# Kernel optimization log

Hardware: AMD Instinct MI355X
Metric: run time of the kernel (lower is better)

## Reference

```python
import jax, jax.numpy as jnp
import numpy as np

D_MODEL = 1024
N_HEADS = 16
HDIM = D_MODEL // N_HEADS
IMP_EPS = 1e-6


def setup_inputs() -> dict:
    key = jax.random.key(0)
    ks = jax.random.split(key, 7)
    B, T_q, T_kv, N_s = 2, 2048, 256, 16
    scale = 1.0 / np.sqrt(D_MODEL)
    return {
        "query": jax.random.normal(ks[0], (B, T_q, D_MODEL), dtype=jnp.float32),
        "key_value": jax.random.normal(ks[1], (B, T_kv, N_s, D_MODEL), dtype=jnp.float32),
        "imp_weights": jax.random.uniform(ks[2], (B, N_s), dtype=jnp.float32),
        "W_q": jax.random.normal(ks[3], (D_MODEL, D_MODEL), dtype=jnp.float32) * scale,
        "W_k": jax.random.normal(ks[4], (D_MODEL, D_MODEL), dtype=jnp.float32) * scale,
        "W_v": jax.random.normal(ks[5], (D_MODEL, D_MODEL), dtype=jnp.float32) * scale,
        "W_o": jax.random.normal(ks[6], (D_MODEL, D_MODEL), dtype=jnp.float32) * scale,
    }


def _split_heads(x):
    # [B, T, D] -> [B, h, T, d]
    B, T, _ = x.shape
    return x.reshape(B, T, N_HEADS, HDIM).transpose(0, 2, 1, 3)


def reference(query, key_value, imp_weights, W_q, W_k, W_v, W_o):
    # CAU_MultiheadCrossAttention.forward with 4D key_value (sensor axis).
    B, T_q, D = query.shape
    _, T_kv, N_s, _ = key_value.shape
    kv = key_value.reshape(B, T_kv * N_s, D)  # flatten sensor axis into source length S

    qh = _split_heads(query @ W_q.T)   # [B,h,T_q,d]  (nn.Linear: x @ W.T)
    kh = _split_heads(kv @ W_k.T)      # [B,h,S,d]
    vh = _split_heads(kv @ W_v.T)      # [B,h,S,d]

    # importance: [B,N_s] -> tiled over T_kv -> [B, S], log-clamped additive mask
    imp_full = jnp.broadcast_to(imp_weights[:, None, :], (B, T_kv, N_s)).reshape(B, T_kv * N_s)
    log_imp = jnp.log(jnp.clip(imp_full, IMP_EPS, None)).astype(qh.dtype)  # [B,S]

    scores = jnp.einsum("bhqd,bhkd->bhqk", qh, kh) / np.sqrt(HDIM).astype(np.float32)
    scores = scores + log_imp[:, None, None, :]
    attn = jax.nn.softmax(scores, axis=-1)
    y = jnp.einsum("bhqk,bhkd->bhqd", attn, vh)  # [B,h,T_q,d]

    y = y.transpose(0, 2, 1, 3).reshape(B, T_q, D)  # merge heads
    return y @ W_o.T
```

## Files before the change

kernel.cpp:

```cpp
#include <hip/hip_runtime.h>
#include <hip/hip_bf16.h>

typedef __bf16    bf16x8_t __attribute__((ext_vector_type(8)));
typedef __bf16    bf16x4_t __attribute__((ext_vector_type(4)));
typedef float     f32x4_t  __attribute__((ext_vector_type(4)));
typedef _Float16  f16x8_t  __attribute__((ext_vector_type(8)));

static __device__ __forceinline__ f32x4_t mfma16(bf16x8_t a, bf16x8_t b, f32x4_t c) {
    return __builtin_amdgcn_mfma_f32_16x16x32_bf16(a, b, c, 0, 0, 0);
}

static __device__ __forceinline__ float redsum16(float v) {
#pragma unroll
    for (int off = 1; off < 16; off <<= 1) v += __shfl_xor(v, off);
    return v;
}

static __device__ __forceinline__ void async16(const __bf16* g, __bf16* l) {
    __builtin_amdgcn_global_load_lds(
        (const __attribute__((address_space(1))) unsigned int*)g,
        (__attribute__((address_space(3))) unsigned int*)l, 16, 0, 0);
}

__global__ __launch_bounds__(256) void f2b_multi(const float* __restrict__ q,
                                                 const float* __restrict__ kv,
                                                 const float* __restrict__ wq,
                                                 const float* __restrict__ wk,
                                                 const float* __restrict__ wv,
                                                 const float* __restrict__ wo,
                                                 __bf16* __restrict__ qb,
                                                 __bf16* __restrict__ kvb,
                                                 __bf16* __restrict__ wqb,
                                                 __bf16* __restrict__ wkvb,
                                                 __bf16* __restrict__ wob,
                                                 float qscale) {
    int i = blockIdx.x * 256 + threadIdx.x;
    const float* src; __bf16* dst; int base; float scale = 1.0f;
    if (i < 1048576)      { src = q;  dst = qb;   base = 0; }
    else if (i < 3145728) { src = kv; dst = kvb;  base = 1048576; }
    else if (i < 3407872) { src = wq; dst = wqb;  base = 3145728; scale = qscale; }
    else if (i < 3670016) { src = wk; dst = wkvb; base = 3407872; }
    else if (i < 3932160) { src = wv; dst = wkvb + 1048576; base = 3670016; }
    else                  { src = wo; dst = wob;  base = 3932160; }
    int j = i - base;
    float4 v = reinterpret_cast<const float4*>(src)[j];
    bf16x4_t o;
    o[0] = (__bf16)(v.x * scale); o[1] = (__bf16)(v.y * scale);
    o[2] = (__bf16)(v.z * scale); o[3] = (__bf16)(v.w * scale);
    reinterpret_cast<bf16x4_t*>(dst)[j] = o;
}

__global__ __launch_bounds__(256) void proj_kernel(const __bf16* __restrict__ qb,
                                                   const __bf16* __restrict__ wqb,
                                                   const __bf16* __restrict__ kvb,
                                                   const __bf16* __restrict__ wkvb,
                                                   __bf16* __restrict__ Qp,
                                                   __bf16* __restrict__ Khd,
                                                   __bf16* __restrict__ Vhd,
                                                   const float* __restrict__ imp) {
    __shared__ __bf16 As[128 * 32];
    __shared__ __bf16 Bs[128 * 32];
    __shared__ __bf16 Es[2][4096];

    const int gid = blockIdx.x;
    const __bf16 *A, *B;
    long m0, n0;
    int mode;
    if (gid < 256) {
        m0 = (long)(gid >> 3) * 128; n0 = (long)(gid & 7) * 128;
        A = qb; B = wqb; mode = 0;
    } else {
        int g2 = gid - 256;
        m0 = (long)(g2 >> 4) * 128; n0 = (long)(g2 & 15) * 128;
        A = kvb; B = wkvb; mode = (n0 < 1024) ? 1 : 2;
    }

    const int t    = threadIdx.x;
    const int w    = t >> 6;
    const int lane = t & 63;
    const int quad = lane >> 4;
    const int mn   = lane & 15;
    const int wm   = (w & 1) * 64;
    const int wn   = (w >> 1) * 64;

    const int  srow = t >> 2;
    const int  scol = (t & 3) * 8;
    const __bf16* gA = A + (m0 + srow) * 1024 + scol;
    const __bf16* gB = B + (n0 + srow) * 1024 + scol;

    f32x4_t acc[4][4];
#pragma unroll
    for (int i = 0; i < 4; i++)
#pragma unroll
        for (int j = 0; j < 4; j++) acc[i][j] = (f32x4_t){0.f, 0.f, 0.f, 0.f};

    for (int k0 = 0; k0 < 1024; k0 += 32) {
        __syncthreads();
        async16(gA + k0,              &As[t * 8]);
        async16(gA + 64 * 1024 + k0,  &As[2048 + t * 8]);
        async16(gB + k0,              &Bs[t * 8]);
        async16(gB + 64 * 1024 + k0,  &Bs[2048 + t * 8]);
        __syncthreads();

        bf16x8_t af[4], bf[4];
#pragma unroll
        for (int i = 0; i < 4; i++)
            af[i] = *(const bf16x8_t*)&As[(wm + i * 16 + mn) * 32 + quad * 8];
#pragma unroll
        for (int j = 0; j < 4; j++)
            bf[j] = *(const bf16x8_t*)&Bs[(wn + j * 16 + mn) * 32 + quad * 8];
#pragma unroll
        for (int i = 0; i < 4; i++)
#pragma unroll
            for (int j = 0; j < 4; j++) acc[i][j] = mfma16(af[i], bf[j], acc[i][j]);
    }

    __syncthreads();
    __bf16* stg = (w == 0) ? As : (w == 1) ? Bs : Es[w - 2];

    if (mode != 2) {
#pragma unroll
        for (int i = 0; i < 4; i++)
#pragma unroll
            for (int j = 0; j < 4; j++)
#pragma unroll
                for (int r = 0; r < 4; r++) {
                    int sl = i * 16 + quad * 4 + r;
                    int d  = j * 16 + mn;
                    stg[sl * 64 + (((d >> 3) ^ (sl & 7)) * 8) + (d & 7)] =
                        (__bf16)acc[i][j][r];
                }
    } else {
        const int b_ = (int)((m0 + wm) >> 12);
#pragma unroll
        for (int r = 0; r < 4; r++) {
            float scl = fmaxf(imp[b_ * 16 + quad * 4 + r], 1e-6f);
#pragma unroll
            for (int j = 0; j < 4; j++) {
                bf16x4_t pk;
#pragma unroll
                for (int i = 0; i < 4; i++) pk[i] = (__bf16)(acc[i][j][r] * scl);
                int d  = j * 16 + mn;
                int p0 = (quad * 4 + r) * 4;
                *(bf16x4_t*)&stg[d * 64 + (((p0 >> 3) ^ (d & 7)) * 8) + (p0 & 7)] = pk;
            }
        }
    }

    if (mode == 0) {
        __bf16* Cg = Qp + (m0 + wm) * 1024 + (n0 + wn);
#pragma unroll
        for (int it = 0; it < 8; it++) {
            int rowL = it * 8 + (lane >> 3);
            int cb   = lane & 7;
            bf16x8_t vv = *(const bf16x8_t*)&stg[rowL * 64 + ((cb ^ (rowL & 7)) * 8)];
            *(bf16x8_t*)&Cg[(long)rowL * 1024 + cb * 8] = vv;
        }
    } else {
        const int b_    = (int)((m0 + wm) >> 12);
        const int sbase = (int)((m0 + wm) & 4095);
        __bf16* dst;
        if (mode == 1) {
            int h_ = (int)((n0 + wn) >> 6);
            dst = Khd + (long)(b_ * 16 + h_) * 262144 + (long)sbase * 64;
        } else {
            int h_ = (int)((n0 + wn) >> 6) - 16;
            dst = Vhd + (long)(b_ * 16 + h_) * 262144 + (long)(sbase >> 6) * 4096;
        }
#pragma unroll
        for (int it = 0; it < 8; it++) {
            int rowL = it * 8 + (lane >> 3);
            int cb   = lane & 7;
            bf16x8_t vv = *(const bf16x8_t*)&stg[rowL * 64 + ((cb ^ (rowL & 7)) * 8)];
            *(bf16x8_t*)&dst[rowL * 64 + cb * 8] = vv;
        }
    }
}

__global__ __launch_bounds__(256, 4) void attn_kernel(const __bf16* __restrict__ Qp,
                                                      const __bf16* __restrict__ Kh,
                                                      const __bf16* __restrict__ Vh,
                                                      const float* __restrict__ imp,
                                                      _Float16* __restrict__ Op,
                                                      float* __restrict__ Lp) {
    const int gid = blockIdx.x;
    const int qt  = (gid >> 3) & 15;
    const int sp  = (gid >> 7) & 1;
    const int bh  = ((gid >> 8) << 3) | (gid & 7);
    const int b   = bh >> 4;
    const int h   = bh & 15;
    const int t    = threadIdx.x;
    const int w    = t >> 6;
    const int lane = t & 63;
    const int quad = lane >> 4;
    const int mn   = lane & 15;

    __shared__ __bf16 Ks[2][64 * 64];
    __shared__ __bf16 Vs[64 * 64];
    __shared__ __bf16 Ps[4][32 * 64];

    const long qrow0 = (long)b * 2048 + qt * 128 + w * 32;
    const __bf16* Kb = Kh + (long)bh * 262144;
    const __bf16* Vb = Vh + (long)bh * 262144;

    const int r8 = lane >> 3;
    const int cs = (lane & 7) ^ r8;
    const int soff    = r8 * 64 + cs * 8;
    const int srcoff0 = (0 * 4 + w) * 512 + soff;
    const int srcoff1 = (1 * 4 + w) * 512 + soff;

    bf16x8_t aq[2][2];
#pragma unroll
    for (int rt = 0; rt < 2; rt++)
#pragma unroll
        for (int x = 0; x < 2; x++)
            aq[rt][x] = *(const bf16x8_t*)&Qp[(qrow0 + rt * 16 + mn) * 1024 + h * 64 + x * 32 + quad * 8];

    const float impc = fmaxf(imp[b * 16 + mn], 1e-6f);

    float lpart[2][4];
    f32x4_t o[2][4];
#pragma unroll
    for (int rt = 0; rt < 2; rt++)
#pragma unroll
        for (int r = 0; r < 4; r++) lpart[rt][r] = 0.f;
#pragma unroll
    for (int rt = 0; rt < 2; rt++)
#pragma unroll
        for (int dt = 0; dt < 4; dt++) o[rt][dt] = (f32x4_t){0.f, 0.f, 0.f, 0.f};

    const int st0 = sp * 32;

    async16(Kb + (long)st0 * 4096 + srcoff0, &Ks[0][(0 * 4 + w) * 512]);
    async16(Kb + (long)st0 * 4096 + srcoff1, &Ks[0][(1 * 4 + w) * 512]);

    for (int it = 0; it < 32; ++it) {
        const int st  = st0 + it;
        const int cur = it & 1;

        __syncthreads();

        async16(Vb + (long)st * 4096 + srcoff0,       &Vs[(0 * 4 + w) * 512]);
        async16(Vb + (long)st * 4096 + srcoff1,       &Vs[(1 * 4 + w) * 512]);
        async16(Kb + (long)(st + 1) * 4096 + srcoff0, &Ks[cur ^ 1][(0 * 4 + w) * 512]);
        async16(Kb + (long)(st + 1) * 4096 + srcoff1, &Ks[cur ^ 1][(1 * 4 + w) * 512]);

        const __bf16* Kc = &Ks[cur][0];
        f32x4_t sc[2][4];
#pragma unroll
        for (int rt = 0; rt < 2; rt++)
#pragma unroll
            for (int ct = 0; ct < 4; ct++) sc[rt][ct] = (f32x4_t){0.f, 0.f, 0.f, 0.f};
#pragma unroll
        for (int ct = 0; ct < 4; ct++) {
            int s  = ct * 16 + mn;
            int c0 = (quad ^ (s & 7)) * 8;
            bf16x8_t bk0 = *(const bf16x8_t*)&Kc[s * 64 + c0];
            bf16x8_t bk1 = *(const bf16x8_t*)&Kc[s * 64 + (c0 ^ 32)];
#pragma unroll
            for (int rt = 0; rt < 2; rt++) {
                sc[rt][ct] = mfma16(aq[rt][0], bk0, sc[rt][ct]);
                sc[rt][ct] = mfma16(aq[rt][1], bk1, sc[rt][ct]);
            }
        }

#pragma unroll
        for (int rt = 0; rt < 2; rt++)
#pragma unroll
            for (int r = 0; r < 4; r++) {
                float p0 = __builtin_amdgcn_exp2f(sc[rt][0][r]);
                float p1 = __builtin_amdgcn_exp2f(sc[rt][1][r]);
                float p2 = __builtin_amdgcn_exp2f(sc[rt][2][r]);
                float p3 = __builtin_amdgcn_exp2f(sc[rt][3][r]);
                lpart[rt][r] += (p0 + p1) + (p2 + p3);
                bf16x4_t pk;
                pk[0] = (__bf16)p0; pk[1] = (__bf16)p1;
                pk[2] = (__bf16)p2; pk[3] = (__bf16)p3;
                int row = rt * 16 + quad * 4 + r;
                *(bf16x4_t*)&Ps[w][row * 64 + (((mn >> 1) ^ (row & 7)) * 8) + (mn & 1) * 4] = pk;
            }

        __syncthreads();

        {
            bf16x8_t bv0[4], bv1[4];
#pragma unroll
            for (int dt = 0; dt < 4; dt++) {
                int d  = dt * 16 + mn;
                int c0 = (quad ^ (d & 7)) * 8;
                bv0[dt] = *(const bf16x8_t*)&Vs[d * 64 + c0];
                bv1[dt] = *(const bf16x8_t*)&Vs[d * 64 + (c0 ^ 32)];
            }
#pragma unroll
            for (int rt = 0; rt < 2; rt++) {
                int arow = rt * 16 + mn;
                bf16x8_t ap0 = *(const bf16x8_t*)&Ps[w][arow * 64 + ((quad ^ (mn & 7)) * 8)];
                bf16x8_t ap1 = *(const bf16x8_t*)&Ps[w][arow * 64 + (((4 + quad) ^ (mn & 7)) * 8)];
#pragma unroll
                for (int dt = 0; dt < 4; dt++) {
                    o[rt][dt] = mfma16(ap0, bv0[dt], o[rt][dt]);
                    o[rt][dt] = mfma16(ap1, bv1[dt], o[rt][dt]);
                }
            }
        }
    }

#pragma unroll
    for (int rt = 0; rt < 2; rt++)
#pragma unroll
        for (int r = 0; r < 4; r++) {
            float l = redsum16(lpart[rt][r] * impc);
            long row = qrow0 + rt * 16 + quad * 4 + r;
            if (mn == 0) Lp[((long)sp * 4096 + row) * 16 + h] = l;
#pragma unroll
            for (int dt = 0; dt < 4; dt++)
                Op[((long)sp * 4096 + row) * 1024 + h * 64 + dt * 16 + mn] =
                    (_Float16)o[rt][dt][r];
        }
}

__global__ __launch_bounds__(256) void combine_kernel(const _Float16* __restrict__ Op,
                                                      const float* __restrict__ Lp,
                                                      __bf16* __restrict__ Y) {
    int tid = blockIdx.x * 256 + threadIdx.x;
    int row = tid >> 7;
    int cg  = tid & 127;
    int h   = cg >> 3;
    f16x8_t o0 = *(const f16x8_t*)&Op[(long)row * 1024 + cg * 8];
    f16x8_t o1 = *(const f16x8_t*)&Op[(long)(4096 + row) * 1024 + cg * 8];
    float inv = 1.0f / (Lp[row * 16 + h] + Lp[(4096 + row) * 16 + h]);
    bf16x8_t y;
#pragma unroll
    for (int j = 0; j < 8; j++) y[j] = (__bf16)(((float)o0[j] + (float)o1[j]) * inv);
    *(bf16x8_t*)&Y[(long)row * 1024 + cg * 8] = y;
}

__global__ __launch_bounds__(256) void gemm_out_kernel(const __bf16* __restrict__ A,
                                                       const __bf16* __restrict__ B,
                                                       float* __restrict__ P) {
    __shared__ __bf16 As[128 * 32];
    __shared__ __bf16 Bs[128 * 32];

    const int  kh = blockIdx.x >> 3;
    const long n0 = (long)(blockIdx.x & 7) * 128;
    const long m0 = (long)blockIdx.y * 128;
    const int  kb = kh * 512;
    float* C = P + (long)kh * 4194304;

    const int t    = threadIdx.x;
    const int w    = t >> 6;
    const int lane = t & 63;
    const int quad = lane >> 4;
    const int mn   = lane & 15;
    const int wm   = (w & 1) * 64;
    const int wn   = (w >> 1) * 64;

    const int  srow = t >> 2;
    const int  scol = (t & 3) * 8;
    const __bf16* gA = A + (m0 + srow) * 1024 + kb + scol;
    const __bf16* gB = B + (n0 + srow) * 1024 + kb + scol;

    f32x4_t acc[4][4];
#pragma unroll
    for (int i = 0; i < 4; i++)
#pragma unroll
        for (int j = 0; j < 4; j++) acc[i][j] = (f32x4_t){0.f, 0.f, 0.f, 0.f};

    for (int k0 = 0; k0 < 512; k0 += 32) {
        __syncthreads();
        async16(gA + k0,             &As[t * 8]);
        async16(gA + 64 * 1024 + k0, &As[2048 + t * 8]);
        async16(gB + k0,             &Bs[t * 8]);
        async16(gB + 64 * 1024 + k0, &Bs[2048 + t * 8]);
        __syncthreads();

        bf16x8_t af[4], bf[4];
#pragma unroll
        for (int i = 0; i < 4; i++)
            af[i] = *(const bf16x8_t*)&As[(wm + i * 16 + mn) * 32 + quad * 8];
#pragma unroll
        for (int j = 0; j < 4; j++)
            bf[j] = *(const bf16x8_t*)&Bs[(wn + j * 16 + mn) * 32 + quad * 8];
#pragma unroll
        for (int i = 0; i < 4; i++)
#pragma unroll
            for (int j = 0; j < 4; j++) acc[i][j] = mfma16(af[i], bf[j], acc[i][j]);
    }

#pragma unroll
    for (int i = 0; i < 4; i++)
#pragma unroll
        for (int j = 0; j < 4; j++)
#pragma unroll
            for (int r = 0; r < 4; r++) {
                long row = m0 + wm + i * 16 + quad * 4 + r;
                long col = n0 + wn + j * 16 + mn;
                C[row * 1024 + col] = acc[i][j][r];
            }
}

__global__ __launch_bounds__(256) void combine2_kernel(const float* __restrict__ P0,
                                                       const float* __restrict__ P1,
                                                       float* __restrict__ out) {
    int i = blockIdx.x * 256 + threadIdx.x;
    float4 a = reinterpret_cast<const float4*>(P0)[i];
    float4 b = reinterpret_cast<const float4*>(P1)[i];
    float4 c; c.x = a.x + b.x; c.y = a.y + b.y; c.z = a.z + b.z; c.w = a.w + b.w;
    reinterpret_cast<float4*>(out)[i] = c;
}

extern "C" void kernel_launch(void* const* d_in, const int* in_sizes, int n_in,
                              void* d_out, int out_size, void* d_ws, size_t ws_size,
                              hipStream_t stream) {
    const float* q_f  = (const float*)d_in[0];
    const float* kv_f = (const float*)d_in[1];
    const float* imp  = (const float*)d_in[2];
    const float* wq_f = (const float*)d_in[3];
    const float* wk_f = (const float*)d_in[4];
    const float* wv_f = (const float*)d_in[5];
    const float* wo_f = (const float*)d_in[6];

    char* ws = (char*)d_ws;
    const size_t MB = 1ull << 20;
    __bf16*   qb    = (__bf16*)(ws + 0);
    __bf16*   kvb   = (__bf16*)(ws + 8 * MB);
    __bf16*   wqb   = (__bf16*)(ws + 24 * MB);
    __bf16*   wkvb  = (__bf16*)(ws + 26 * MB);
    _Float16* Opart = (_Float16*)(ws + 0);
    float*    Lpart = (float*)(ws + 16 * MB);
    __bf16*   Yb    = (__bf16*)(ws + 17 * MB);
    __bf16*   wob   = (__bf16*)(ws + 30 * MB);
    __bf16*   Qp    = (__bf16*)(ws + 32 * MB);
    __bf16*   Khd   = (__bf16*)(ws + 40 * MB);
    __bf16*   Vhd   = (__bf16*)(ws + 56 * MB);
    float*    Gp    = (float*)(ws + 40 * MB);

    const float QSCALE = 0.125f * 1.4426950408889634f;

    f2b_multi<<<16384, 256, 0, stream>>>(q_f, kv_f, wq_f, wk_f, wv_f, wo_f,
                                         qb, kvb, wqb, wkvb, wob, QSCALE);

    proj_kernel<<<1280, 256, 0, stream>>>(qb, wqb, kvb, wkvb, Qp, Khd, Vhd, imp);

    attn_kernel<<<1024, 256, 0, stream>>>(Qp, Khd, Vhd, imp, Opart, Lpart);
    combine_kernel<<<2048, 256, 0, stream>>>(Opart, Lpart, Yb);

    gemm_out_kernel<<<dim3(16, 32), 256, 0, stream>>>(Yb, wob, Gp);
    combine2_kernel<<<4096, 256, 0, stream>>>(Gp, Gp + 4194304, (float*)d_out);
}
```

Baseline: 290.9 us.

## Halve attention query tile to 64 rows, double grid, add MFMA priority hints

```diff
diff --git a/kernel.cpp b/kernel.cpp
--- a/kernel.cpp
+++ b/kernel.cpp
@@ -177,16 +177,16 @@
     }
 }
 
-__global__ __launch_bounds__(256, 4) void attn_kernel(const __bf16* __restrict__ Qp,
+__global__ __launch_bounds__(256, 5) void attn_kernel(const __bf16* __restrict__ Qp,
                                                       const __bf16* __restrict__ Kh,
                                                       const __bf16* __restrict__ Vh,
                                                       const float* __restrict__ imp,
                                                       _Float16* __restrict__ Op,
                                                       float* __restrict__ Lp) {
     const int gid = blockIdx.x;
-    const int qt  = (gid >> 3) & 15;
-    const int sp  = (gid >> 7) & 1;
-    const int bh  = ((gid >> 8) << 3) | (gid & 7);
+    const int qt  = (gid >> 3) & 31;
+    const int sp  = (gid >> 8) & 1;
+    const int bh  = ((gid >> 9) << 3) | (gid & 7);
     const int b   = bh >> 4;
     const int h   = bh & 15;
     const int t    = threadIdx.x;
@@ -197,9 +197,9 @@
 
     __shared__ __bf16 Ks[2][64 * 64];
     __shared__ __bf16 Vs[64 * 64];
-    __shared__ __bf16 Ps[4][32 * 64];
-
-    const long qrow0 = (long)b * 2048 + qt * 128 + w * 32;
+    __shared__ __bf16 Ps[4][16 * 64];
+
+    const long qrow0 = (long)b * 2048 + qt * 64 + w * 16;
     const __bf16* Kb = Kh + (long)bh * 262144;
     const __bf16* Vb = Vh + (long)bh * 262144;
 
@@ -209,25 +209,19 @@
     const int srcoff0 = (0 * 4 + w) * 512 + soff;
     const int srcoff1 = (1 * 4 + w) * 512 + soff;
 
-    bf16x8_t aq[2][2];
-#pragma unroll
-    for (int rt = 0; rt < 2; rt++)
-#pragma unroll
-        for (int x = 0; x < 2; x++)
-            aq[rt][x] = *(const bf16x8_t*)&Qp[(qrow0 + rt * 16 + mn) * 1024 + h * 64 + x * 32 + quad * 8];
+    bf16x8_t aq[2];
+#pragma unroll
+    for (int x = 0; x < 2; x++)
+        aq[x] = *(const bf16x8_t*)&Qp[(qrow0 + mn) * 1024 + h * 64 + x * 32 + quad * 8];
 
     const float impc = fmaxf(imp[b * 16 + mn], 1e-6f);
 
-    float lpart[2][4];
-    f32x4_t o[2][4];
-#pragma unroll
-    for (int rt = 0; rt < 2; rt++)
-#pragma unroll
-        for (int r = 0; r < 4; r++) lpart[rt][r] = 0.f;
-#pragma unroll
-    for (int rt = 0; rt < 2; rt++)
-#pragma unroll
-        for (int dt = 0; dt < 4; dt++) o[rt][dt] = (f32x4_t){0.f, 0.f, 0.f, 0.f};
+    float lpart[4];
+    f32x4_t o[4];
+#pragma unroll
+    for (int r = 0; r < 4; r++) lpart[r] = 0.f;
+#pragma unroll
+    for (int dt = 0; dt < 4; dt++) o[dt] = (f32x4_t){0.f, 0.f, 0.f, 0.f};
 
     const int st0 = sp * 32;
 
@@ -246,39 +240,34 @@
         async16(Kb + (long)(st + 1) * 4096 + srcoff1, &Ks[cur ^ 1][(1 * 4 + w) * 512]);
 
         const __bf16* Kc = &Ks[cur][0];
-        f32x4_t sc[2][4];
-#pragma unroll
-        for (int rt = 0; rt < 2; rt++)
-#pragma unroll
-            for (int ct = 0; ct < 4; ct++) sc[rt][ct] = (f32x4_t){0.f, 0.f, 0.f, 0.f};
+        f32x4_t sc[4];
+#pragma unroll
+        for (int ct = 0; ct < 4; ct++) sc[ct] = (f32x4_t){0.f, 0.f, 0.f, 0.f};
+        __builtin_amdgcn_s_setprio(1);
 #pragma unroll
         for (int ct = 0; ct < 4; ct++) {
             int s  = ct * 16 + mn;
             int c0 = (quad ^ (s & 7)) * 8;
             bf16x8_t bk0 = *(const bf16x8_t*)&Kc[s * 64 + c0];
             bf16x8_t bk1 = *(const bf16x8_t*)&Kc[s * 64 + (c0 ^ 32)];
-#pragma unroll
-            for (int rt = 0; rt < 2; rt++) {
-                sc[rt][ct] = mfma16(aq[rt][0], bk0, sc[rt][ct]);
-                sc[rt][ct] = mfma16(aq[rt][1], bk1, sc[rt][ct]);
-            }
-        }
-
-#pragma unroll
-        for (int rt = 0; rt < 2; rt++)
-#pragma unroll
-            for (int r = 0; r < 4; r++) {
-                float p0 = __builtin_amdgcn_exp2f(sc[rt][0][r]);
-                float p1 = __builtin_amdgcn_exp2f(sc[rt][1][r]);
-                float p2 = __builtin_amdgcn_exp2f(sc[rt][2][r]);
-                float p3 = __builtin_amdgcn_exp2f(sc[rt][3][r]);
-                lpart[rt][r] += (p0 + p1) + (p2 + p3);
-                bf16x4_t pk;
-                pk[0] = (__bf16)p0; pk[1] = (__bf16)p1;
-                pk[2] = (__bf16)p2; pk[3] = (__bf16)p3;
-                int row = rt * 16 + quad * 4 + r;
-                *(bf16x4_t*)&Ps[w][row * 64 + (((mn >> 1) ^ (row & 7)) * 8) + (mn & 1) * 4] = pk;
-            }
+            sc[ct] = mfma16(aq[0], bk0, sc[ct]);
+            sc[ct] = mfma16(aq[1], bk1, sc[ct]);
+        }
+        __builtin_amdgcn_s_setprio(0);
+
+#pragma unroll
+        for (int r = 0; r < 4; r++) {
+            float p0 = __builtin_amdgcn_exp2f(sc[0][r]);
+            float p1 = __builtin_amdgcn_exp2f(sc[1][r]);
+            float p2 = __builtin_amdgcn_exp2f(sc[2][r]);
+            float p3 = __builtin_amdgcn_exp2f(sc[3][r]);
+            lpart[r] += (p0 + p1) + (p2 + p3);
+            bf16x4_t pk;
+            pk[0] = (__bf16)p0; pk[1] = (__bf16)p1;
+            pk[2] = (__bf16)p2; pk[3] = (__bf16)p3;
+            int row = quad * 4 + r;
+            *(bf16x4_t*)&Ps[w][row * 64 + (((mn >> 1) ^ (row & 7)) * 8) + (mn & 1) * 4] = pk;
+        }
 
         __syncthreads();
 
@@ -291,32 +280,28 @@
                 bv0[dt] = *(const bf16x8_t*)&Vs[d * 64 + c0];
                 bv1[dt] = *(const bf16x8_t*)&Vs[d * 64 + (c0 ^ 32)];
             }
-#pragma unroll
-            for (int rt = 0; rt < 2; rt++) {
-                int arow = rt * 16 + mn;
-                bf16x8_t ap0 = *(const bf16x8_t*)&Ps[w][arow * 64 + ((quad ^ (mn & 7)) * 8)];
-                bf16x8_t ap1 = *(const bf16x8_t*)&Ps[w][arow * 64 + (((4 + quad) ^ (mn & 7)) * 8)];
-#pragma unroll
-                for (int dt = 0; dt < 4; dt++) {
-                    o[rt][dt] = mfma16(ap0, bv0[dt], o[rt][dt]);
-                    o[rt][dt] = mfma16(ap1, bv1[dt], o[rt][dt]);
-                }
+            bf16x8_t ap0 = *(const bf16x8_t*)&Ps[w][mn * 64 + ((quad ^ (mn & 7)) * 8)];
+            bf16x8_t ap1 = *(const bf16x8_t*)&Ps[w][mn * 64 + (((4 + quad) ^ (mn & 7)) * 8)];
+            __builtin_amdgcn_s_setprio(1);
+#pragma unroll
+            for (int dt = 0; dt < 4; dt++) {
+                o[dt] = mfma16(ap0, bv0[dt], o[dt]);
+                o[dt] = mfma16(ap1, bv1[dt], o[dt]);
             }
-        }
-    }
-
-#pragma unroll
-    for (int rt = 0; rt < 2; rt++)
-#pragma unroll
-        for (int r = 0; r < 4; r++) {
-            float l = redsum16(lpart[rt][r] * impc);
-            long row = qrow0 + rt * 16 + quad * 4 + r;
-            if (mn == 0) Lp[((long)sp * 4096 + row) * 16 + h] = l;
-#pragma unroll
-            for (int dt = 0; dt < 4; dt++)
-                Op[((long)sp * 4096 + row) * 1024 + h * 64 + dt * 16 + mn] =
-                    (_Float16)o[rt][dt][r];
-        }
+            __builtin_amdgcn_s_setprio(0);
+        }
+    }
+
+#pragma unroll
+    for (int r = 0; r < 4; r++) {
+        float l = redsum16(lpart[r] * impc);
+        long row = qrow0 + quad * 4 + r;
+        if (mn == 0) Lp[((long)sp * 4096 + row) * 16 + h] = l;
+#pragma unroll
+        for (int dt = 0; dt < 4; dt++)
+            Op[((long)sp * 4096 + row) * 1024 + h * 64 + dt * 16 + mn] =
+                (_Float16)o[dt][r];
+    }
 }
 
 __global__ __launch_bounds__(256) void combine_kernel(const _Float16* __restrict__ Op,
@@ -442,7 +427,7 @@
 
     proj_kernel<<<1280, 256, 0, stream>>>(qb, wqb, kvb, wkvb, Qp, Khd, Vhd, imp);
 
-    attn_kernel<<<1024, 256, 0, stream>>>(Qp, Khd, Vhd, imp, Opart, Lpart);
+    attn_kernel<<<2048, 256, 0, stream>>>(Qp, Khd, Vhd, imp, Opart, Lpart);
     combine_kernel<<<2048, 256, 0, stream>>>(Opart, Lpart, Yb);
 
     gemm_out_kernel<<<dim3(16, 32), 256, 0, stream>>>(Yb, wob, Gp);
```

Result: slower. 309.9 us (+6.5%).
